# Kernel tuning notes

Measured on AMD Instinct MI355X. Metric: run time of the kernel, lower is better.

## Reference

```python
import jax, jax.numpy as jnp
import numpy as np


def _conv3(x, w):
    # 3x3 conv, stride 1, padding 1 (SAME), NCHW/OIHW
    return jax.lax.conv_general_dilated(
        x, w, window_strides=(1, 1), padding=((1, 1), (1, 1)),
        dimension_numbers=("NCHW", "OIHW", "NCHW"))


def setup_inputs() -> dict:
    key = jax.random.key(0)
    ks = jax.random.split(key, 10)
    B, C, H, W = 16, 64, 128, 128
    NL = 4
    inp = {
        "x0": jax.random.normal(ks[0], (B, C, H, W), dtype=jnp.float32),
        "spa_mask": jax.random.uniform(ks[1], (B, 1, H, W), dtype=jnp.float32),
        # uniform noise in (0,1) for gumbel; bounded away from 0 like the torch retry loop
        "gumbels": jax.random.uniform(ks[2], (1, C, NL, 2), dtype=jnp.float32,
                                      minval=1e-6, maxval=1.0 - 1e-6),
        "ch_mask_param": jax.random.uniform(ks[3], (1, C, NL, 2), dtype=jnp.float32),
        "w0": jax.random.normal(ks[4], (C, C, 3, 3), dtype=jnp.float32) * 0.05,
        "w1": jax.random.normal(ks[5], (C, C, 3, 3), dtype=jnp.float32) * 0.05,
        "w2": jax.random.normal(ks[6], (C, C, 3, 3), dtype=jnp.float32) * 0.05,
        "w3": jax.random.normal(ks[7], (C, C, 3, 3), dtype=jnp.float32) * 0.05,
        "wc": jax.random.normal(ks[8], (C, C * NL, 1, 1), dtype=jnp.float32) * 0.05,
        "bc": jax.random.normal(ks[9], (C,), dtype=jnp.float32) * 0.05,
    }
    return inp


def reference(x0, spa_mask, gumbels, ch_mask_param, w0, w1, w2, w3, wc, bc):
    tau = 1.0
    g = -jnp.log(-jnp.log(gumbels))
    ch_mask = jax.nn.softmax((ch_mask_param + g) / tau, axis=3)  # (1,C,NL,2)
    ws = [w0, w1, w2, w3]
    outs = []
    fea = x0
    for i in range(4):
        m_d = ch_mask[:, :, i, 0][:, :, None, None]  # dense-path channel gate (1,C,1,1)
        m_s = ch_mask[:, :, i, 1][:, :, None, None]  # sparse-path channel gate
        if i == 0:
            fea = _conv3(fea, ws[0])
            fea = fea * m_s * spa_mask + fea * m_d
        else:
            fea_d = _conv3(fea * m_d, ws[i])
            fea_s = _conv3(fea * m_s, ws[i])
            fea = (fea_d * m_s * spa_mask + fea_d * m_d
                   + fea_s * m_s * spa_mask + fea_s * m_d * spa_mask)
        fea = jax.nn.relu(fea)
        outs.append(fea)
    cat = jnp.concatenate(outs, axis=1)  # (B, 4C, H, W)
    out = jnp.einsum("oc,bchw->bohw", wc[:, :, 0, 0], cat) + bc[None, :, None, None]
    return (out, ch_mask)
```

## Files before the change

### kernel.cpp

```cpp
#include <hip/hip_runtime.h>
#include <math.h>

#define B_ 16
#define C_ 64
#define H_ 128
#define W_ 128
#define HW_ (H_*W_)
#define OUT_ELEMS 16777216

#define CHM_B    0
#define PWA_B    2048
#define AH_B     34816
#define FEA_B(s) (550912u + (size_t)(s)*33554432u)

#define A_S0   0
#define A_S(s) (36864 + ((s)-1)*73728)

#define SUBT 14040

typedef __attribute__((ext_vector_type(4))) short  v4s;
typedef __attribute__((ext_vector_type(8))) short  v8s;
typedef __attribute__((ext_vector_type(4))) float  v4f;

__device__ __forceinline__ ushort f2bf(float f) {
    unsigned u = __builtin_bit_cast(unsigned, f);
    unsigned r = u + 0x7FFFu + ((u >> 16) & 1u);
    return (ushort)(r >> 16);
}

__global__ __launch_bounds__(64) void mask_kernel(
    const float* __restrict__ gum, const float* __restrict__ par,
    float* __restrict__ chm, float* __restrict__ out_tail)
{
    int c = threadIdx.x;
    #pragma unroll
    for (int i = 0; i < 4; ++i) {
        int base = (c*4 + i)*2;
        float g0 = -logf(-logf(gum[base]));
        float g1 = -logf(-logf(gum[base+1]));
        float a0 = par[base] + g0, a1 = par[base+1] + g1;
        float mx = fmaxf(a0, a1);
        float e0 = expf(a0 - mx), e1 = expf(a1 - mx);
        float inv = 1.0f / (e0 + e1);
        float m0 = e0*inv, m1 = e1*inv;
        chm[base] = m0; chm[base+1] = m1;
        out_tail[base] = m0; out_tail[base+1] = m1;
    }
}

__global__ __launch_bounds__(256) void prep_kernel(
    const float* __restrict__ w0, const float* __restrict__ w1,
    const float* __restrict__ w2, const float* __restrict__ w3,
    const float* __restrict__ wc, const float* __restrict__ chm,
    ushort* __restrict__ AH, ushort* __restrict__ pwA)
{
    int idx = blockIdx.x*256 + threadIdx.x;
    if (idx < 36864) {
        int blk = idx >> 11;
        int r3  = idx & 2047;
        int oc = r3 >> 5, icl = r3 & 31;
        int cc = blk / 9, t = blk - 9*cc;
        int ic = cc*32 + icl;
        AH[idx] = f2bf(w0[(oc*64 + ic)*9 + t]);
    } else if (idx < 258048) {
        int j = idx - 36864;
        int s = 1 + j / 73728;
        int r = j % 73728;
        int blk = r >> 12;
        int r3  = r & 4095;
        int ocM = r3 >> 5, icl = r3 & 31;
        int cc = blk / 9, t = blk - 9*cc;
        int ic = cc*32 + icl;
        int oc = ocM >> 1, set = ocM & 1;
        const float* wsrc = (s == 1) ? w1 : (s == 2 ? w2 : w3);
        AH[idx] = f2bf(wsrc[(oc*64 + ic)*9 + t] * chm[(ic*4 + s)*2 + set]);
    } else {
        int r = idx - 258048;
        pwA[r] = f2bf(wc[r]);
    }
}

template<int NSETS, bool INF32>
__global__ __launch_bounds__(256, 2) void conv_bf16(
    const void* __restrict__ inv, const ushort* __restrict__ A,
    const float* __restrict__ chm, const float* __restrict__ spa,
    ushort* __restrict__ feaOut, int stage)
{
    constexpr int MOC = 64*NSETS;
    constexpr int MT  = MOC/32;
    __shared__ __align__(16) ushort sB[2*SUBT];

    const int tid  = threadIdx.x;
    const int lane = tid & 63, wave = tid >> 6;
    const int wrow = wave >> 1, wcol = wave & 1;
    const int q = lane >> 4, ln16 = lane & 15;
    const int wk = (blockIdx.x & 7)*256 + (blockIdx.x >> 3);
    const int h = wk & 127, b = wk >> 7;

    v4f acc[MT][4];
    #pragma unroll
    for (int m = 0; m < MT; ++m)
        #pragma unroll
        for (int n = 0; n < 4; ++n) acc[m][n] = (v4f){0.f, 0.f, 0.f, 0.f};

    int aRow[MT];
    #pragma unroll
    for (int m = 0; m < MT; ++m)
        aRow[m] = (wrow*(MOC/2) + m*16 + ln16)*32 + q*8;

    v8s stg[12];
    v4f stgF[24];
    v8s af[4][MT];

    auto issue = [&](int c) {
        const int ic0 = c*32;
        #pragma unroll
        for (int it = 0; it < 6; ++it) {
            int i  = it*256 + tid;
            int ry = i >> 9;
            int r  = i & 511;
            int ic = r >> 4, wv = r & 15;
            int gh = h - 1 + ry;
            if constexpr (INF32) {
                v4f a0 = (v4f){0.f,0.f,0.f,0.f}, a1 = a0;
                if ((unsigned)gh < 128u) {
                    const float* s = (const float*)inv +
                        ((size_t)((b*C_ + ic0 + ic)*H_ + gh)*W_ + wv*8);
                    a0 = *(const v4f*)(const void*)s;
                    a1 = *(const v4f*)(const void*)(s + 4);
                }
                stgF[(c*6+it)*2] = a0; stgF[(c*6+it)*2+1] = a1;
            } else {
                v8s v = (v8s){0,0,0,0,0,0,0,0};
                if ((unsigned)gh < 128u)
                    v = *(const v8s*)(const void*)((const ushort*)inv +
                        ((size_t)((b*C_ + ic0 + ic)*H_ + gh)*W_ + wv*8));
                stg[c*6+it] = v;
            }
        }
    };
    auto scatter = [&](int c) {
        ushort* sBc = sB + c*SUBT;
        #pragma unroll
        for (int it = 0; it < 6; ++it) {
            int i  = it*256 + tid;
            int ry = i >> 9;
            int r  = i & 511;
            int ic = r >> 4, wv = r & 15;
            int colBase = ry*130 + wv*8 + 1;
            ushort vals[8];
            if constexpr (INF32) {
                #pragma unroll
                for (int j = 0; j < 4; ++j) {
                    vals[j]   = f2bf(stgF[(c*6+it)*2][j]);
                    vals[4+j] = f2bf(stgF[(c*6+it)*2+1][j]);
                }
            } else {
                #pragma unroll
                for (int j = 0; j < 8; ++j) vals[j] = (ushort)stg[c*6+it][j];
            }
            #pragma unroll
            for (int j = 0; j < 8; ++j) {
                int colIdx = colBase + j;
                int s3 = (colIdx >> 3) & 7;
                sBc[colIdx*36 + (ic ^ (s3 << 2))] = vals[j];
            }
        }
    };
    auto prolog = [&]() {
        #pragma unroll
        for (int tp = 0; tp < 3; ++tp)
            #pragma unroll
            for (int m = 0; m < MT; ++m)
                af[tp][m] = *(const v8s*)(const void*)(A + tp*MOC*32 + aRow[m]);
    };
    auto computeAll = [&]() {
        #pragma unroll
        for (int tt = 0; tt < 18; ++tt) {
            if (tt < 15) {
                #pragma unroll
                for (int m = 0; m < MT; ++m)
                    af[(tt+3)&3][m] = *(const v8s*)(const void*)(A + (tt+3)*MOC*32 + aRow[m]);
            }
            const int c  = tt/9, t = tt - 9*c;
            const int ky = t/3, kx = t - 3*(t/3);
            const ushort* sBc = sB + c*SUBT;
            #pragma unroll
            for (int nt = 0; nt < 4; ++nt) {
                int colIdx = ky*130 + wcol*64 + nt*16 + ln16 + kx;
                int s3 = (colIdx >> 3) & 7;
                int base = colIdx*36 + ((q ^ (s3 >> 1)) << 3);
                int lo = base + ((s3 & 1) << 2);
                int hi = base + (((s3 & 1) ^ 1) << 2);
                v4s va = *(const v4s*)(const void*)(sBc + lo);
                v4s vb = *(const v4s*)(const void*)(sBc + hi);
                v8s bf = __builtin_shufflevector(va, vb, 0, 1, 2, 3, 4, 5, 6, 7);
                #pragma unroll
                for (int m = 0; m < MT; ++m)
                    acc[m][nt] = __builtin_amdgcn_mfma_f32_16x16x32_bf16(af[tt&3][m], bf, acc[m][nt], 0, 0, 0);
            }
        }
    };

    issue(0);
    issue(1);
    prolog();
    if (tid < 216) {
        int colSel = tid / 36;
        int icz    = tid - colSel*36;
        int ry     = colSel >> 1;
        int colIdx = ry*130 + ((colSel & 1) ? 129 : 0);
        sB[colIdx*36 + icz] = 0;
        sB[SUBT + colIdx*36 + icz] = 0;
    }
    scatter(0);
    scatter(1);
    __syncthreads();
    computeAll();

    const float* spaRow = &spa[b*HW_ + h*W_];
    #pragma unroll
    for (int nt = 0; nt < 4; ++nt) {
        int px = wcol*64 + nt*16 + ln16;
        float sp = spaRow[px];
        #pragma unroll
        for (int m = 0; m < MT; ++m) {
            if constexpr (NSETS == 2) {
                #pragma unroll
                for (int rp = 0; rp < 2; ++rp) {
                    int oc = wrow*32 + m*8 + q*2 + rp;
                    float md = chm[(oc*4 + stage)*2 + 0];
                    float ms = chm[(oc*4 + stage)*2 + 1];
                    float f = acc[m][nt][2*rp]*(ms*sp + md)
                            + acc[m][nt][2*rp+1]*((ms + md)*sp);
                    feaOut[((size_t)(b*C_ + oc)*H_ + h)*W_ + px] = f2bf(fmaxf(f, 0.f));
                }
            } else {
                #pragma unroll
                for (int r = 0; r < 4; ++r) {
                    int oc = wrow*32 + m*16 + q*4 + r;
                    float md = chm[(oc*4 + stage)*2 + 0];
                    float ms = chm[(oc*4 + stage)*2 + 1];
                    float f = acc[m][nt][r]*(ms*sp + md);
                    feaOut[((size_t)(b*C_ + oc)*H_ + h)*W_ + px] = f2bf(fmaxf(f, 0.f));
                }
            }
        }
    }
}

__global__ __launch_bounds__(256, 2) void pw_final(
    const ushort* __restrict__ fea, const ushort* __restrict__ pwA,
    const float* __restrict__ bc, float* __restrict__ out)
{
    __shared__ __align__(16) ushort sF[64*260];

    const int tid  = threadIdx.x;
    const int lane = tid & 63, wave = tid >> 6;
    const int wrow = wave >> 1, wcol = wave & 1;
    const int q = lane >> 4, ln16 = lane & 15;
    const int half = blockIdx.x & 1;
    const int h = (blockIdx.x >> 1) & 127;
    const int b = blockIdx.x >> 8;
    const int px0 = half*64;

    {
        v8s stg[8];
        #pragma unroll
        for (int it = 0; it < 8; ++it) {
            int i  = it*256 + tid;
            int s  = i >> 9;
            int r  = i & 511;
            int ic = r >> 3, pxv = r & 7;
            stg[it] = *(const v8s*)(const void*)(
                fea + (size_t)s*OUT_ELEMS + ((size_t)(b*C_ + ic)*H_ + h)*W_ + px0 + pxv*8);
        }
        #pragma unroll
        for (int it = 0; it < 8; ++it) {
            int i  = it*256 + tid;
            int s  = i >> 9;
            int r  = i & 511;
            int ic = r >> 3, pxv = r & 7;
            int kS = (s*64 + ic) ^ ((pxv & 3) << 3);
            ushort* dst = &sF[(pxv*8)*260 + kS];
            #pragma unroll
            for (int j = 0; j < 8; ++j) dst[j*260] = (ushort)stg[it][j];
        }
    }
    __syncthreads();

    v4f acc[2][2];
    #pragma unroll
    for (int m = 0; m < 2; ++m)
        #pragma unroll
        for (int n = 0; n < 2; ++n) acc[m][n] = (v4f){0.f, 0.f, 0.f, 0.f};

    #pragma unroll
    for (int ks = 0; ks < 8; ++ks) {
        v8s a[2];
        #pragma unroll
        for (int m = 0; m < 2; ++m)
            a[m] = *(const v8s*)(const void*)(pwA + (wrow*32 + m*16 + ln16)*256 + ks*32 + q*8);
        #pragma unroll
        for (int n = 0; n < 2; ++n) {
            int px = wcol*32 + n*16 + ln16;
            int swz = (px >> 3) & 3;
            v4s va = *(const v4s*)(const void*)(sF + px*260 + ks*32 + ((q ^ swz) << 3));
            v4s vb = *(const v4s*)(const void*)(sF + px*260 + ks*32 + ((q ^ swz) << 3) + 4);
            v8s bf = __builtin_shufflevector(va, vb, 0, 1, 2, 3, 4, 5, 6, 7);
            #pragma unroll
            for (int m = 0; m < 2; ++m)
                acc[m][n] = __builtin_amdgcn_mfma_f32_16x16x32_bf16(a[m], bf, acc[m][n], 0, 0, 0);
        }
    }

    #pragma unroll
    for (int n = 0; n < 2; ++n) {
        int px = px0 + wcol*32 + n*16 + ln16;
        #pragma unroll
        for (int m = 0; m < 2; ++m)
            #pragma unroll
            for (int r = 0; r < 4; ++r) {
                int o = wrow*32 + m*16 + q*4 + r;
                out[((size_t)(b*C_ + o)*H_ + h)*W_ + px] = acc[m][n][r] + bc[o];
            }
    }
}

extern "C" void kernel_launch(void* const* d_in, const int* in_sizes, int n_in,
                              void* d_out, int out_size, void* d_ws, size_t ws_size,
                              hipStream_t stream)
{
    const float* x0  = (const float*)d_in[0];
    const float* spa = (const float*)d_in[1];
    const float* gum = (const float*)d_in[2];
    const float* par = (const float*)d_in[3];
    const float* w0  = (const float*)d_in[4];
    const float* w1  = (const float*)d_in[5];
    const float* w2  = (const float*)d_in[6];
    const float* w3  = (const float*)d_in[7];
    const float* wc  = (const float*)d_in[8];
    const float* bc  = (const float*)d_in[9];
    float* out = (float*)d_out;
    char*  ws  = (char*)d_ws;

    float*  chm = (float*)(ws + CHM_B);
    ushort* pwA = (ushort*)(ws + PWA_B);
    ushort* AH  = (ushort*)(ws + AH_B);
    ushort* fea0 = (ushort*)(ws + FEA_B(0));
    ushort* fea1 = (ushort*)(ws + FEA_B(1));
    ushort* fea2 = (ushort*)(ws + FEA_B(2));
    ushort* fea3 = (ushort*)(ws + FEA_B(3));

    mask_kernel<<<1, 64, 0, stream>>>(gum, par, chm, out + OUT_ELEMS);
    prep_kernel<<<1072, 256, 0, stream>>>(w0, w1, w2, w3, wc, chm, AH, pwA);

    conv_bf16<1, true ><<<2048, 256, 0, stream>>>(x0,   AH + A_S0,  chm, spa, fea0, 0);
    conv_bf16<2, false><<<2048, 256, 0, stream>>>(fea0, AH + A_S(1), chm, spa, fea1, 1);
    conv_bf16<2, false><<<2048, 256, 0, stream>>>(fea1, AH + A_S(2), chm, spa, fea2, 2);
    conv_bf16<2, false><<<2048, 256, 0, stream>>>(fea2, AH + A_S(3), chm, spa, fea3, 3);

    pw_final<<<4096, 256, 0, stream>>>(fea0, pwA, bc, out);
}
```

Baseline: 388.5 us.

## Compute two output rows per block in stage 1-3 convolutions

```diff
diff --git a/kernel.cpp b/kernel.cpp
--- a/kernel.cpp
+++ b/kernel.cpp
@@ -15,8 +15,6 @@
 
 #define A_S0   0
 #define A_S(s) (36864 + ((s)-1)*73728)
-
-#define SUBT 14040
 
 typedef __attribute__((ext_vector_type(4))) short  v4s;
 typedef __attribute__((ext_vector_type(8))) short  v8s;
@@ -80,47 +78,47 @@
     }
 }
 
-template<int NSETS, bool INF32>
+template<int NSETS, bool INF32, int ROWS>
 __global__ __launch_bounds__(256, 2) void conv_bf16(
     const void* __restrict__ inv, const ushort* __restrict__ A,
     const float* __restrict__ chm, const float* __restrict__ spa,
     ushort* __restrict__ feaOut, int stage)
 {
-    constexpr int MOC = 64*NSETS;
-    constexpr int MT  = MOC/32;
-    __shared__ __align__(16) ushort sB[2*SUBT];
+    constexpr int MOC  = 64*NSETS;
+    constexpr int MT   = MOC/32;
+    constexpr int RP2  = ROWS + 2;
+    constexpr int SUBT = RP2*130*36;
+    constexpr int ITS  = RP2*2;
+    constexpr int HB   = H_/ROWS;
+    constexpr int NBLK = B_*HB;
+    extern __shared__ ushort sB[];
 
     const int tid  = threadIdx.x;
     const int lane = tid & 63, wave = tid >> 6;
     const int wrow = wave >> 1, wcol = wave & 1;
     const int q = lane >> 4, ln16 = lane & 15;
-    const int wk = (blockIdx.x & 7)*256 + (blockIdx.x >> 3);
-    const int h = wk & 127, b = wk >> 7;
-
-    v4f acc[MT][4];
-    #pragma unroll
-    for (int m = 0; m < MT; ++m)
-        #pragma unroll
-        for (int n = 0; n < 4; ++n) acc[m][n] = (v4f){0.f, 0.f, 0.f, 0.f};
+    const int wk = (blockIdx.x & 7)*(NBLK/8) + (blockIdx.x >> 3);
+    const int h0 = (wk % HB)*ROWS;
+    const int b  = wk / HB;
 
     int aRow[MT];
     #pragma unroll
     for (int m = 0; m < MT; ++m)
         aRow[m] = (wrow*(MOC/2) + m*16 + ln16)*32 + q*8;
 
-    v8s stg[12];
-    v4f stgF[24];
+    v8s stg[2*ITS];
+    v4f stgF[4*ITS];
     v8s af[4][MT];
 
     auto issue = [&](int c) {
         const int ic0 = c*32;
         #pragma unroll
-        for (int it = 0; it < 6; ++it) {
+        for (int it = 0; it < ITS; ++it) {
             int i  = it*256 + tid;
             int ry = i >> 9;
             int r  = i & 511;
             int ic = r >> 4, wv = r & 15;
-            int gh = h - 1 + ry;
+            int gh = h0 - 1 + ry;
             if constexpr (INF32) {
                 v4f a0 = (v4f){0.f,0.f,0.f,0.f}, a1 = a0;
                 if ((unsigned)gh < 128u) {
@@ -129,20 +127,20 @@
                     a0 = *(const v4f*)(const void*)s;
                     a1 = *(const v4f*)(const void*)(s + 4);
                 }
-                stgF[(c*6+it)*2] = a0; stgF[(c*6+it)*2+1] = a1;
+                stgF[(c*ITS+it)*2] = a0; stgF[(c*ITS+it)*2+1] = a1;
             } else {
                 v8s v = (v8s){0,0,0,0,0,0,0,0};
                 if ((unsigned)gh < 128u)
                     v = *(const v8s*)(const void*)((const ushort*)inv +
                         ((size_t)((b*C_ + ic0 + ic)*H_ + gh)*W_ + wv*8));
-                stg[c*6+it] = v;
+                stg[c*ITS+it] = v;
             }
         }
     };
     auto scatter = [&](int c) {
         ushort* sBc = sB + c*SUBT;
         #pragma unroll
-        for (int it = 0; it < 6; ++it) {
+        for (int it = 0; it < ITS; ++it) {
             int i  = it*256 + tid;
             int ry = i >> 9;
             int r  = i & 511;
@@ -152,12 +150,12 @@
             if constexpr (INF32) {
                 #pragma unroll
                 for (int j = 0; j < 4; ++j) {
-                    vals[j]   = f2bf(stgF[(c*6+it)*2][j]);
-                    vals[4+j] = f2bf(stgF[(c*6+it)*2+1][j]);
+                    vals[j]   = f2bf(stgF[(c*ITS+it)*2][j]);
+                    vals[4+j] = f2bf(stgF[(c*ITS+it)*2+1][j]);
                 }
             } else {
                 #pragma unroll
-                for (int j = 0; j < 8; ++j) vals[j] = (ushort)stg[c*6+it][j];
+                for (int j = 0; j < 8; ++j) vals[j] = (ushort)stg[c*ITS+it][j];
             }
             #pragma unroll
             for (int j = 0; j < 8; ++j) {
@@ -174,20 +172,45 @@
             for (int m = 0; m < MT; ++m)
                 af[tp][m] = *(const v8s*)(const void*)(A + tp*MOC*32 + aRow[m]);
     };
-    auto computeAll = [&]() {
-        #pragma unroll
-        for (int tt = 0; tt < 18; ++tt) {
-            if (tt < 15) {
-                #pragma unroll
-                for (int m = 0; m < MT; ++m)
-                    af[(tt+3)&3][m] = *(const v8s*)(const void*)(A + (tt+3)*MOC*32 + aRow[m]);
-            }
-            const int c  = tt/9, t = tt - 9*c;
-            const int ky = t/3, kx = t - 3*(t/3);
-            const ushort* sBc = sB + c*SUBT;
-            #pragma unroll
-            for (int nt = 0; nt < 4; ++nt) {
-                int colIdx = ky*130 + wcol*64 + nt*16 + ln16 + kx;
+
+    issue(0);
+    issue(1);
+    prolog();
+    for (int e = tid; e < RP2*72; e += 256) {
+        int colSel = e / 36;
+        int icz    = e - colSel*36;
+        int rr     = colSel >> 1;
+        int colIdx = rr*130 + ((colSel & 1) ? 129 : 0);
+        sB[colIdx*36 + icz] = 0;
+        sB[SUBT + colIdx*36 + icz] = 0;
+    }
+    scatter(0);
+    scatter(1);
+    __syncthreads();
+
+    v4f acc[MT][ROWS][4];
+    #pragma unroll
+    for (int m = 0; m < MT; ++m)
+        #pragma unroll
+        for (int r = 0; r < ROWS; ++r)
+            #pragma unroll
+            for (int n = 0; n < 4; ++n) acc[m][r][n] = (v4f){0.f,0.f,0.f,0.f};
+
+    #pragma unroll
+    for (int tt = 0; tt < 18; ++tt) {
+        if (tt < 15) {
+            #pragma unroll
+            for (int m = 0; m < MT; ++m)
+                af[(tt+3)&3][m] = *(const v8s*)(const void*)(A + (tt+3)*MOC*32 + aRow[m]);
+        }
+        const int c  = tt/9, t = tt - 9*c;
+        const int ky = t/3, kx = t - 3*(t/3);
+        const ushort* sBc = sB + c*SUBT;
+        #pragma unroll
+        for (int nt = 0; nt < 4; ++nt) {
+            #pragma unroll
+            for (int r = 0; r < ROWS; ++r) {
+                int colIdx = (ky + r)*130 + wcol*64 + nt*16 + ln16 + kx;
                 int s3 = (colIdx >> 3) & 7;
                 int base = colIdx*36 + ((q ^ (s3 >> 1)) << 3);
                 int lo = base + ((s3 & 1) << 2);
@@ -197,52 +220,40 @@
                 v8s bf = __builtin_shufflevector(va, vb, 0, 1, 2, 3, 4, 5, 6, 7);
                 #pragma unroll
                 for (int m = 0; m < MT; ++m)
-                    acc[m][nt] = __builtin_amdgcn_mfma_f32_16x16x32_bf16(af[tt&3][m], bf, acc[m][nt], 0, 0, 0);
-            }
-        }
-    };
-
-    issue(0);
-    issue(1);
-    prolog();
-    if (tid < 216) {
-        int colSel = tid / 36;
-        int icz    = tid - colSel*36;
-        int ry     = colSel >> 1;
-        int colIdx = ry*130 + ((colSel & 1) ? 129 : 0);
-        sB[colIdx*36 + icz] = 0;
-        sB[SUBT + colIdx*36 + icz] = 0;
-    }
-    scatter(0);
-    scatter(1);
-    __syncthreads();
-    computeAll();
-
-    const float* spaRow = &spa[b*HW_ + h*W_];
-    #pragma unroll
-    for (int nt = 0; nt < 4; ++nt) {
-        int px = wcol*64 + nt*16 + ln16;
-        float sp = spaRow[px];
-        #pragma unroll
-        for (int m = 0; m < MT; ++m) {
-            if constexpr (NSETS == 2) {
-                #pragma unroll
-                for (int rp = 0; rp < 2; ++rp) {
-                    int oc = wrow*32 + m*8 + q*2 + rp;
-                    float md = chm[(oc*4 + stage)*2 + 0];
-                    float ms = chm[(oc*4 + stage)*2 + 1];
-                    float f = acc[m][nt][2*rp]*(ms*sp + md)
-                            + acc[m][nt][2*rp+1]*((ms + md)*sp);
-                    feaOut[((size_t)(b*C_ + oc)*H_ + h)*W_ + px] = f2bf(fmaxf(f, 0.f));
-                }
-            } else {
-                #pragma unroll
-                for (int r = 0; r < 4; ++r) {
-                    int oc = wrow*32 + m*16 + q*4 + r;
-                    float md = chm[(oc*4 + stage)*2 + 0];
-                    float ms = chm[(oc*4 + stage)*2 + 1];
-                    float f = acc[m][nt][r]*(ms*sp + md);
-                    feaOut[((size_t)(b*C_ + oc)*H_ + h)*W_ + px] = f2bf(fmaxf(f, 0.f));
+                    acc[m][r][nt] = __builtin_amdgcn_mfma_f32_16x16x32_bf16(af[tt&3][m], bf, acc[m][r][nt], 0, 0, 0);
+            }
+        }
+    }
+
+    #pragma unroll
+    for (int r = 0; r < ROWS; ++r) {
+        const int h = h0 + r;
+        const float* spaRow = &spa[b*HW_ + h*W_];
+        #pragma unroll
+        for (int nt = 0; nt < 4; ++nt) {
+            int px = wcol*64 + nt*16 + ln16;
+            float sp = spaRow[px];
+            #pragma unroll
+            for (int m = 0; m < MT; ++m) {
+                if constexpr (NSETS == 2) {
+                    #pragma unroll
+                    for (int rp = 0; rp < 2; ++rp) {
+                        int oc = wrow*32 + m*8 + q*2 + rp;
+                        float md = chm[(oc*4 + stage)*2 + 0];
+                        float ms = chm[(oc*4 + stage)*2 + 1];
+                        float f = acc[m][r][nt][2*rp]*(ms*sp + md)
+                                + acc[m][r][nt][2*rp+1]*((ms + md)*sp);
+                        feaOut[((size_t)(b*C_ + oc)*H_ + h)*W_ + px] = f2bf(fmaxf(f, 0.f));
+                    }
+                } else {
+                    #pragma unroll
+                    for (int rr4 = 0; rr4 < 4; ++rr4) {
+                        int oc = wrow*32 + m*16 + q*4 + rr4;
+                        float md = chm[(oc*4 + stage)*2 + 0];
+                        float ms = chm[(oc*4 + stage)*2 + 1];
+                        float f = acc[m][r][nt][rr4]*(ms*sp + md);
+                        feaOut[((size_t)(b*C_ + oc)*H_ + h)*W_ + px] = f2bf(fmaxf(f, 0.f));
+                    }
                 }
             }
         }
@@ -352,13 +363,16 @@
     ushort* fea2 = (ushort*)(ws + FEA_B(2));
     ushort* fea3 = (ushort*)(ws + FEA_B(3));
 
+    const size_t lds1 = 2u*(1+2)*130*36*2;
+    const size_t lds2 = 2u*(2+2)*130*36*2;
+
     mask_kernel<<<1, 64, 0, stream>>>(gum, par, chm, out + OUT_ELEMS);
     prep_kernel<<<1072, 256, 0, stream>>>(w0, w1, w2, w3, wc, chm, AH, pwA);
 
-    conv_bf16<1, true ><<<2048, 256, 0, stream>>>(x0,   AH + A_S0,  chm, spa, fea0, 0);
-    conv_bf16<2, false><<<2048, 256, 0, stream>>>(fea0, AH + A_S(1), chm, spa, fea1, 1);
-    conv_bf16<2, false><<<2048, 256, 0, stream>>>(fea1, AH + A_S(2), chm, spa, fea2, 2);
-    conv_bf16<2, false><<<2048, 256, 0, stream>>>(fea2, AH + A_S(3), chm, spa, fea3, 3);
+    conv_bf16<1, true , 1><<<2048, 256, lds1, stream>>>(x0,   AH + A_S0,  chm, spa, fea0, 0);
+    conv_bf16<2, false, 2><<<1024, 256, lds2, stream>>>(fea0, AH + A_S(1), chm, spa, fea1, 1);
+    conv_bf16<2, false, 2><<<1024, 256, lds2, stream>>>(fea1, AH + A_S(2), chm, spa, fea2, 2);
+    conv_bf16<2, false, 2><<<1024, 256, lds2, stream>>>(fea2, AH + A_S(3), chm, spa, fea3, 3);
 
     pw_final<<<4096, 256, 0, stream>>>(fea0, pwA, bc, out);
 }
```

After: 464.4 us. 19.5% more time.
